# Performance work log

Hardware: AMD Instinct MI355X
Metric: run time of the kernel (lower is better)

The kernel has to match this reference:

```python
import jax, jax.numpy as jnp
import numpy as np


def _log_g(x):
    # numerically stable log of g(x) = where(x>=0, x+0.5, sigmoid(x))
    return jnp.where(x >= 0, jnp.log(jax.nn.relu(x) + 0.5), -jax.nn.softplus(-x))


def setup_inputs() -> dict:
    key = jax.random.key(0)
    k1, k2, k3, k4 = jax.random.split(key, 4)
    B, T, D = 4, 4096, 1024
    Di = 2 * D  # dim_inner = int(dim * expansion_factor), expansion_factor = 2.0
    x = jax.random.normal(k1, (B, T, D), dtype=jnp.float32)
    prev_hidden = jax.random.uniform(k2, (B, Di), dtype=jnp.float32)  # positive carry state
    # torch Linear(dim, 2*dim_inner, bias=False): stored here pre-transposed as [D, 2*Di]
    W_hg = jax.random.normal(k3, (D, 2 * Di), dtype=jnp.float32) * (1.0 / np.sqrt(D))
    # out_proj Linear(dim_inner, dim, bias=False): stored pre-transposed as [Di, D]
    W_out = jax.random.normal(k4, (Di, D), dtype=jnp.float32) * (1.0 / np.sqrt(Di))
    return {"x": x, "prev_hidden": prev_hidden, "W_hg": W_hg, "W_out": W_out}


def reference(x, prev_hidden, W_hg, W_out):
    # x: [B, T, D]; prev_hidden: [B, Di] (positive)
    T = x.shape[1]
    hg = jnp.einsum('btd,de->bte', x, W_hg)          # [B, T, 2*Di]
    hidden, gate = jnp.split(hg, 2, axis=-1)          # each [B, T, Di]

    # Heinsen log-space affine scan: h_t = (1 - z_t) * h_{t-1} + z_t * g(hidden_t)
    log_coeffs = -jax.nn.softplus(gate)               # log(1 - sigmoid(gate))
    log_values = -jax.nn.softplus(-gate) + _log_g(hidden)  # log(sigmoid(gate)) + log g(hidden)

    # prepend carry state
    prev_log = jnp.clip(jnp.log(jnp.clip(prev_hidden, 1e-8, None)), -30.0, None)[:, None]  # [B,1,Di]
    log_values = jnp.concatenate([prev_log, log_values], axis=1)      # [B, T+1, Di]
    log_coeffs = jnp.pad(log_coeffs, ((0, 0), (1, 0), (0, 0)))        # [B, T+1, Di]

    a_star = jnp.cumsum(log_coeffs, axis=1)
    h = jnp.exp(a_star + jax.lax.cumlogsumexp(log_values - a_star, axis=1))  # [B, T+1, Di]
    h = h[:, -T:]                                     # drop carry slot

    next_hidden = h[:, -1]                            # [B, Di]
    out = jnp.einsum('bte,ed->btd', h, W_out)         # [B, T, D]
    return (out, next_hidden)
```

## Files before the change

kernel.cpp:

```cpp
#include <hip/hip_runtime.h>
#include <cstdio>

#define T_LEN 4096
#define B_SZ  4
#define D_IN  1024
#define DI    2048
#define MM    16384
#define NC    32
#define CHL   128

typedef __attribute__((ext_vector_type(8))) __bf16 bf16x8;
typedef __attribute__((ext_vector_type(4))) float  f32x4;
typedef __attribute__((ext_vector_type(8))) unsigned short u16x8;

__device__ __forceinline__ unsigned short f2bf(float f){
  unsigned u = __builtin_bit_cast(unsigned, f);
  u += 0x7fffu + ((u >> 16) & 1u);
  return (unsigned short)(u >> 16);
}
__device__ __forceinline__ float bf2f_lo(unsigned u){
  return __builtin_bit_cast(float, u << 16);
}
__device__ __forceinline__ float bf2f_hi(unsigned u){
  return __builtin_bit_cast(float, u & 0xffff0000u);
}

__device__ __forceinline__ void async16(void* lds, const void* g){
  __builtin_amdgcn_global_load_lds((const __attribute__((address_space(1))) void*)g,
                                   (__attribute__((address_space(3))) void*)lds, 16, 0, 0);
}

__global__ __launch_bounds__(256) void k_convert_x(const float* __restrict__ x,
                                                   unsigned short* __restrict__ xb){
  size_t t = (size_t)blockIdx.x*256 + threadIdx.x;
  const float4* xi = (const float4*)x;
  float4 a = xi[2*t], b = xi[2*t+1];
  u16x8 o;
  o[0]=f2bf(a.x); o[1]=f2bf(a.y); o[2]=f2bf(a.z); o[3]=f2bf(a.w);
  o[4]=f2bf(b.x); o[5]=f2bf(b.y); o[6]=f2bf(b.z); o[7]=f2bf(b.w);
  ((u16x8*)xb)[t] = o;
}

template<int PERM>
__global__ __launch_bounds__(256) void k_transpose(const float* __restrict__ src,
                                                   unsigned short* __restrict__ dst,
                                                   int SK, int SN){
  __shared__ float tile[64][65];
  int n0 = blockIdx.x*64, k0 = blockIdx.y*64;
  #pragma unroll
  for(int it=0; it<16; it++){
    int idx = it*256 + threadIdx.x;
    int kk = idx>>6, nn = idx&63;
    int n = n0+nn;
    int col = PERM ? (((n>>5)<<4) + (n&15) + ((n&16)?2048:0)) : n;
    tile[kk][nn] = src[(size_t)(k0+kk)*SN + col];
  }
  __syncthreads();
  #pragma unroll
  for(int it=0; it<16; it++){
    int idx = it*256 + threadIdx.x;
    int nn = idx>>6, kk = idx&63;
    dst[(size_t)(n0+nn)*SK + k0+kk] = f2bf(tile[kk][nn]);
  }
}

template<int EPI>
__global__ __launch_bounds__(256, 2)
void k_gemm(const unsigned short* __restrict__ A, const unsigned short* __restrict__ Bt,
            float* __restrict__ C0, unsigned short* __restrict__ U0,
            unsigned short* __restrict__ U1, int M, int N, int K){
  __shared__ unsigned short lsA[128*32];
  __shared__ unsigned short lsB[128*32];
  int tid  = threadIdx.x;
  int lane = tid & 63, wave = tid >> 6;
  int wm = wave >> 1, wn = wave & 1;
  int cl = lane & 15, quad = lane >> 4;
  int m0 = blockIdx.y * 128, n0 = blockIdx.x * 128;

  f32x4 acc[4][4];
  #pragma unroll
  for(int i=0;i<4;i++)
    #pragma unroll
    for(int j=0;j<4;j++) acc[i][j] = (f32x4){0.f,0.f,0.f,0.f};

  const unsigned short* gA = A  + (size_t)(m0 + (tid>>2))*K + (tid&3)*8;
  const unsigned short* gB = Bt + (size_t)(n0 + (tid>>2))*K + (tid&3)*8;
  unsigned short* dA = lsA + tid*8;
  unsigned short* dB = lsB + tid*8;

  for(int k0=0; k0<K; k0+=32){
    async16(dA,        gA + k0);
    async16(dA + 2048, gA + (size_t)64*K + k0);
    async16(dB,        gB + k0);
    async16(dB + 2048, gB + (size_t)64*K + k0);
    __syncthreads();
    bf16x8 fa[4], fb[4];
    #pragma unroll
    for(int t2=0;t2<4;t2++){
      fa[t2] = *(const bf16x8*)&lsA[(wm*64 + t2*16 + cl)*32 + quad*8];
      fb[t2] = *(const bf16x8*)&lsB[(wn*64 + t2*16 + cl)*32 + quad*8];
    }
    #pragma unroll
    for(int i=0;i<4;i++)
      #pragma unroll
      for(int j=0;j<4;j++)
        acc[i][j] = __builtin_amdgcn_mfma_f32_16x16x32_bf16(fa[i], fb[j], acc[i][j], 0, 0, 0);
    __syncthreads();
  }

  if(EPI==0){
    #pragma unroll
    for(int i=0;i<4;i++)
      #pragma unroll
      for(int j=0;j<4;j++){
        int n = n0 + wn*64 + j*16 + cl;
        #pragma unroll
        for(int r=0;r<4;r++){
          int m = m0 + wm*64 + i*16 + quad*4 + r;
          C0[(size_t)m*N + n] = acc[i][j][r];
        }
      }
  } else {
    int ibase = ((n0 + wn*64) >> 1) + cl;
    #pragma unroll
    for(int i=0;i<4;i++)
      #pragma unroll
      for(int p=0;p<2;p++){
        f32x4 hh = acc[i][2*p], gg = acc[i][2*p+1];
        int ii = ibase + p*16;
        #pragma unroll
        for(int r=0;r<4;r++){
          int m = m0 + wm*64 + i*16 + quad*4 + r;
          float gate = gg[r], hid = hh[r];
          float e  = __expf(gate);
          float cc = 1.f/(1.f + e);
          float z  = (gate > 80.f) ? 1.f : e*cc;
          float gv = (hid >= 0.f) ? (hid + 0.5f) : (1.f/(1.f + __expf(-hid)));
          U0[(size_t)m*DI + ii] = f2bf(cc);
          U1[(size_t)m*DI + ii] = f2bf(z*gv);
        }
      }
  }
}

__global__ __launch_bounds__(256) void k_scanA(const unsigned* __restrict__ cp,
                                               const unsigned* __restrict__ vp,
                                               float* __restrict__ Ap,
                                               float* __restrict__ Vp){
  int t = blockIdx.x*256 + threadIdx.x;
  int i2 = t & (DI/2 - 1);
  int ch = (t >> 10) & (NC-1);
  int b  = t >> 15;
  size_t base = ((size_t)(b*T_LEN + ch*CHL))*(DI/2) + i2;
  float A0=1.f, V0=0.f, A1=1.f, V1=0.f;
  #pragma unroll 8
  for(int s=0; s<CHL; s++){
    unsigned cu = cp[base], vu = vp[base];
    float c0=bf2f_lo(cu), c1=bf2f_hi(cu), v0=bf2f_lo(vu), v1=bf2f_hi(vu);
    A0 *= c0; V0 = fmaf(c0, V0, v0);
    A1 *= c1; V1 = fmaf(c1, V1, v1);
    base += DI/2;
  }
  size_t o = (size_t)(b*NC + ch)*DI + 2*i2;
  Ap[o] = A0; Ap[o+1] = A1;
  Vp[o] = V0; Vp[o+1] = V1;
}

__global__ __launch_bounds__(256) void k_scanB(const float* __restrict__ prev,
                                               const float* __restrict__ Ap,
                                               const float* __restrict__ Vp,
                                               float* __restrict__ hin){
  int t = blockIdx.x*256 + threadIdx.x;
  int i = t & (DI-1); int b = t >> 11;
  float h = fmaxf(prev[t], 1e-8f);
  for(int ch=0; ch<NC; ch++){
    size_t o = (size_t)(b*NC + ch)*DI + i;
    hin[o] = h;
    h = fmaf(Ap[o], h, Vp[o]);
  }
}

__global__ __launch_bounds__(256) void k_scanC(const unsigned* __restrict__ cp,
                                               unsigned* __restrict__ vp,
                                               const float* __restrict__ hin,
                                               float* __restrict__ nh){
  int t = blockIdx.x*256 + threadIdx.x;
  int i2 = t & (DI/2 - 1);
  int ch = (t >> 10) & (NC-1);
  int b  = t >> 15;
  size_t base = ((size_t)(b*T_LEN + ch*CHL))*(DI/2) + i2;
  size_t ho = (size_t)(b*NC + ch)*DI + 2*i2;
  float h0 = hin[ho], h1 = hin[ho+1];
  #pragma unroll 4
  for(int s=0; s<CHL; s++){
    unsigned cu = cp[base], vu = vp[base];
    h0 = fmaf(bf2f_lo(cu), h0, bf2f_lo(vu));
    h1 = fmaf(bf2f_hi(cu), h1, bf2f_hi(vu));
    vp[base] = (unsigned)f2bf(h0) | ((unsigned)f2bf(h1) << 16);
    base += DI/2;
  }
  if(ch == NC-1){ nh[b*DI + 2*i2] = h0; nh[b*DI + 2*i2 + 1] = h1; }
}

extern "C" void kernel_launch(void* const* d_in, const int* in_sizes, int n_in,
                              void* d_out, int out_size, void* d_ws, size_t ws_size,
                              hipStream_t stream){
  const float* x    = (const float*)d_in[0];
  const float* prev = (const float*)d_in[1];
  const float* Whg  = (const float*)d_in[2];
  const float* Wout = (const float*)d_in[3];
  float* out = (float*)d_out;
  float* nh  = out + (size_t)MM*D_IN;

  const size_t NEED = 116391936;
  if(ws_size < NEED){
    fprintf(stderr, "kernel_launch: ws_size=%zu < needed %zu — aborting launch\n",
            ws_size, NEED);
    return;
  }
  char* ws = (char*)d_ws;
  unsigned short* xb = (unsigned short*)(ws);
  unsigned short* wt = (unsigned short*)(ws + 33554432);
  unsigned short* wo = (unsigned short*)(ws + 41943040);
  unsigned short* v  = (unsigned short*)(ws + 46137344);
  float* Ap  = (float*)(ws + 113246208);
  float* Vp  = (float*)(ws + 114294784);
  float* hin = (float*)(ws + 115343360);
  unsigned short* c = (unsigned short*)d_out;

  k_convert_x<<<8192, 256, 0, stream>>>(x, xb);
  k_transpose<1><<<dim3(64,16), 256, 0, stream>>>(Whg,  wt, 1024, 4096);
  k_transpose<0><<<dim3(16,32), 256, 0, stream>>>(Wout, wo, 2048, 1024);

  k_gemm<1><<<dim3(32,128), 256, 0, stream>>>(xb, wt, nullptr, c, v, MM, 2*DI, D_IN);

  k_scanA<<<512, 256, 0, stream>>>((const unsigned*)c, (const unsigned*)v, Ap, Vp);
  k_scanB<<<32,  256, 0, stream>>>(prev, Ap, Vp, hin);
  k_scanC<<<512, 256, 0, stream>>>((const unsigned*)c, (unsigned*)v, hin, nh);

  k_gemm<0><<<dim3(8,128), 256, 0, stream>>>(v, wo, out, nullptr, nullptr, MM, D_IN, DI);
}
```

Measured before the change: 447.6 us.

## Fuse chunk-scan reduction into GEMM epilogue and swizzle LDS tiles

Removes the separate scanA kernel by computing per-chunk scan products (A, V) inside the first GEMM epilogue, using LDS to combine 4-row segments across waves. This avoids re-reading the bf16 coefficient and value tensors from global memory. It also XOR-swizzles the LDS layout of GEMM tiles to reduce bank conflicts on fragment reads. In exchange it adds an extra barrier and serial 32-step loop for 64 threads in the epilogue, and the scan now composes products in fp32 from unrounded values.

```diff
diff --git a/kernel.cpp b/kernel.cpp
--- a/kernel.cpp
+++ b/kernel.cpp
@@ -68,7 +68,8 @@
 __global__ __launch_bounds__(256, 2)
 void k_gemm(const unsigned short* __restrict__ A, const unsigned short* __restrict__ Bt,
             float* __restrict__ C0, unsigned short* __restrict__ U0,
-            unsigned short* __restrict__ U1, int M, int N, int K){
+            unsigned short* __restrict__ U1, float* __restrict__ Ap,
+            float* __restrict__ Vp, int M, int N, int K){
   __shared__ unsigned short lsA[128*32];
   __shared__ unsigned short lsB[128*32];
   int tid  = threadIdx.x;
@@ -83,10 +84,12 @@
     #pragma unroll
     for(int j=0;j<4;j++) acc[i][j] = (f32x4){0.f,0.f,0.f,0.f};
 
-  const unsigned short* gA = A  + (size_t)(m0 + (tid>>2))*K + (tid&3)*8;
-  const unsigned short* gB = Bt + (size_t)(n0 + (tid>>2))*K + (tid&3)*8;
+  int cs = (tid&3) ^ ((tid>>3)&3);
+  const unsigned short* gA = A  + (size_t)(m0 + (tid>>2))*K + cs*8;
+  const unsigned short* gB = Bt + (size_t)(n0 + (tid>>2))*K + cs*8;
   unsigned short* dA = lsA + tid*8;
   unsigned short* dB = lsB + tid*8;
+  int qa8 = (quad ^ ((cl>>1)&3)) * 8;
 
   for(int k0=0; k0<K; k0+=32){
     async16(dA,        gA + k0);
@@ -97,8 +100,8 @@
     bf16x8 fa[4], fb[4];
     #pragma unroll
     for(int t2=0;t2<4;t2++){
-      fa[t2] = *(const bf16x8*)&lsA[(wm*64 + t2*16 + cl)*32 + quad*8];
-      fb[t2] = *(const bf16x8*)&lsB[(wn*64 + t2*16 + cl)*32 + quad*8];
+      fa[t2] = *(const bf16x8*)&lsA[(wm*64 + t2*16 + cl)*32 + qa8];
+      fb[t2] = *(const bf16x8*)&lsB[(wn*64 + t2*16 + cl)*32 + qa8];
     }
     #pragma unroll
     for(int i=0;i<4;i++)
@@ -121,6 +124,8 @@
         }
       }
   } else {
+    float* lA_f = (float*)lsA;
+    float* lV_f = (float*)lsB;
     int ibase = ((n0 + wn*64) >> 1) + cl;
     #pragma unroll
     for(int i=0;i<4;i++)
@@ -128,6 +133,7 @@
       for(int p=0;p<2;p++){
         f32x4 hh = acc[i][2*p], gg = acc[i][2*p+1];
         int ii = ibase + p*16;
+        float pa = 1.f, pv = 0.f;
         #pragma unroll
         for(int r=0;r<4;r++){
           int m = m0 + wm*64 + i*16 + quad*4 + r;
@@ -136,34 +142,30 @@
           float cc = 1.f/(1.f + e);
           float z  = (gate > 80.f) ? 1.f : e*cc;
           float gv = (hid >= 0.f) ? (hid + 0.5f) : (1.f/(1.f + __expf(-hid)));
+          float vv = z*gv;
           U0[(size_t)m*DI + ii] = f2bf(cc);
-          U1[(size_t)m*DI + ii] = f2bf(z*gv);
+          U1[(size_t)m*DI + ii] = f2bf(vv);
+          pa *= cc;
+          pv = fmaf(cc, pv, vv);
         }
+        int seg = wm*16 + i*4 + quad;
+        int chl = wn*32 + p*16 + cl;
+        lA_f[seg*64 + chl] = pa;
+        lV_f[seg*64 + chl] = pv;
       }
-  }
-}
-
-__global__ __launch_bounds__(256) void k_scanA(const unsigned* __restrict__ cp,
-                                               const unsigned* __restrict__ vp,
-                                               float* __restrict__ Ap,
-                                               float* __restrict__ Vp){
-  int t = blockIdx.x*256 + threadIdx.x;
-  int i2 = t & (DI/2 - 1);
-  int ch = (t >> 10) & (NC-1);
-  int b  = t >> 15;
-  size_t base = ((size_t)(b*T_LEN + ch*CHL))*(DI/2) + i2;
-  float A0=1.f, V0=0.f, A1=1.f, V1=0.f;
-  #pragma unroll 8
-  for(int s=0; s<CHL; s++){
-    unsigned cu = cp[base], vu = vp[base];
-    float c0=bf2f_lo(cu), c1=bf2f_hi(cu), v0=bf2f_lo(vu), v1=bf2f_hi(vu);
-    A0 *= c0; V0 = fmaf(c0, V0, v0);
-    A1 *= c1; V1 = fmaf(c1, V1, v1);
-    base += DI/2;
-  }
-  size_t o = (size_t)(b*NC + ch)*DI + 2*i2;
-  Ap[o] = A0; Ap[o+1] = A1;
-  Vp[o] = V0; Vp[o+1] = V1;
+    __syncthreads();
+    if(tid < 64){
+      float Ac = 1.f, Vc = 0.f;
+      #pragma unroll 8
+      for(int s=0; s<32; s++){
+        float a = lA_f[s*64 + tid], v = lV_f[s*64 + tid];
+        Ac *= a;
+        Vc = fmaf(a, Vc, v);
+      }
+      size_t o = (size_t)(m0 >> 7)*DI + (n0 >> 1) + tid;
+      Ap[o] = Ac; Vp[o] = Vc;
+    }
+  }
 }
 
 __global__ __launch_bounds__(256) void k_scanB(const float* __restrict__ prev,
@@ -232,11 +234,12 @@
   k_transpose<1><<<dim3(64,16), 256, 0, stream>>>(Whg,  wt, 1024, 4096);
   k_transpose<0><<<dim3(16,32), 256, 0, stream>>>(Wout, wo, 2048, 1024);
 
-  k_gemm<1><<<dim3(32,128), 256, 0, stream>>>(xb, wt, nullptr, c, v, MM, 2*DI, D_IN);
-
-  k_scanA<<<512, 256, 0, stream>>>((const unsigned*)c, (const unsigned*)v, Ap, Vp);
+  k_gemm<1><<<dim3(32,128), 256, 0, stream>>>(xb, wt, nullptr, c, v, Ap, Vp,
+                                              MM, 2*DI, D_IN);
+
   k_scanB<<<32,  256, 0, stream>>>(prev, Ap, Vp, hin);
   k_scanC<<<512, 256, 0, stream>>>((const unsigned*)c, (unsigned*)v, hin, nh);
 
-  k_gemm<0><<<dim3(8,128), 256, 0, stream>>>(v, wo, out, nullptr, nullptr, MM, D_IN, DI);
-}
+  k_gemm<0><<<dim3(8,128), 256, 0, stream>>>(v, wo, out, nullptr, nullptr,
+                                             nullptr, nullptr, MM, D_IN, DI);
+}
```

Result: faster. 424.7 us (-5.1%).
